# Optimization experiments

Measured on AMD Instinct MI355X. Metric: run time of the kernel, lower is better.

The kernel has to match this reference:

```python
import jax, jax.numpy as jnp
import numpy as np

N, P, C, H, W = 2, 100, 256, 128, 192
K = 3; KK = K * K; E = C * KK; NH = 8; DH = E // NH; FFN = 2048


def _ln(x, g, b, eps=1e-5):
    m = x.mean(-1, keepdims=True)
    v = ((x - m) ** 2).mean(-1, keepdims=True)
    return (x - m) * jax.lax.rsqrt(v + eps) * g + b


def setup_inputs():
    ks = iter(jax.random.split(jax.random.key(0), 64))
    def rnd(shape, s=1.0):
        return jax.random.normal(next(ks), shape, jnp.float32) * s
    z = lambda *s: jnp.zeros(s, jnp.float32)
    o = lambda *s: jnp.ones(s, jnp.float32)
    return {
        'x': rnd((N, C, H, W)),
        'proposal_feat': rnd((N, P, E)),
        'mask_preds': rnd((N, P, H, W)),
        'ku_dyn_w': rnd((2 * C, C), 0.02), 'ku_dyn_b': z(2 * C),
        'ku_in_w': rnd((2 * C, C), 0.02), 'ku_in_b': z(2 * C),
        'ku_ig_w': rnd((C, C), 0.02), 'ku_ig_b': z(C),
        'ku_ug_w': rnd((C, C), 0.02), 'ku_ug_b': z(C),
        'ku_nin_g': o(C), 'ku_nin_b': z(C),
        'ku_nout_g': o(C), 'ku_nout_b': z(C),
        'ku_inin_g': o(C), 'ku_inin_b': z(C),
        'ku_inout_g': o(C), 'ku_inout_b': z(C),
        'ku_fc_w': rnd((C, C), 0.02), 'ku_fc_b': z(C),
        'ku_fcn_g': o(C), 'ku_fcn_b': z(C),
        'attn_in_w': rnd((3 * E, E), 0.02), 'attn_in_b': z(3 * E),
        'attn_out_w': rnd((E, E), 0.02), 'attn_out_b': z(E),
        'attn_ln_g': o(E), 'attn_ln_b': z(E),
        'ffn_w1': rnd((FFN, C), 0.02), 'ffn_b1': z(FFN),
        'ffn_w2': rnd((C, FFN), 0.02), 'ffn_b2': z(C),
        'ffn_ln_g': o(C), 'ffn_ln_b': z(C),
        'mask_fc_ws': rnd((3, C, C), 0.02),
        'mask_fc_ln_g': o(3, C), 'mask_fc_ln_b': z(3, C),
        'fc_mask_w': rnd((C, C), 0.02), 'fc_mask_b': z(C),
    }


def _forward(x, proposal_feat, mask_preds, ku_dyn_w, ku_dyn_b, ku_in_w, ku_in_b,
             ku_ig_w, ku_ig_b, ku_ug_w, ku_ug_b, ku_nin_g, ku_nin_b, ku_nout_g,
             ku_nout_b, ku_inin_g, ku_inin_b, ku_inout_g, ku_inout_b, ku_fc_w,
             ku_fc_b, ku_fcn_g, ku_fcn_b, attn_in_w, attn_in_b, attn_out_w,
             attn_out_b, attn_ln_g, attn_ln_b, ffn_w1, ffn_b1, ffn_w2, ffn_b2,
             ffn_ln_g, ffn_ln_b, mask_fc_ws, mask_fc_ln_g, mask_fc_ln_b,
             fc_mask_w, fc_mask_b):
    # mask-softmax pooling over proposals: (N,P,H,W) x (N,C,H,W) -> (N,P,C)
    sig = jax.nn.softmax(mask_preds, axis=1)
    x_feat = jnp.einsum('bnhw,bchw->bnc', sig, x)

    # KernelUpdator (gated dynamic kernel update)
    pf = proposal_feat.reshape(N, P, C, KK).transpose(0, 1, 3, 2).reshape(N * P, KK, C)
    upd = x_feat.reshape(N * P, C)
    params = upd @ ku_dyn_w.T + ku_dyn_b            # (NP, 2C)
    p_in, p_out = params[:, :C], params[:, C:]
    inp = pf @ ku_in_w.T + ku_in_b                  # (NP, KK, 2C)
    i_in, i_out = inp[..., :C], inp[..., C:]
    gate = i_in * p_in[:, None, :]                  # (NP, KK, C)
    ig = jax.nn.sigmoid(_ln(gate @ ku_ig_w.T + ku_ig_b, ku_inin_g, ku_inin_b))
    ug = jax.nn.sigmoid(_ln(gate @ ku_ug_w.T + ku_ug_b, ku_nin_g, ku_nin_b))
    p_out = _ln(p_out, ku_nout_g, ku_nout_b)
    i_out = _ln(i_out, ku_inout_g, ku_inout_b)
    feat = ug * p_out[:, None, :] + ig * i_out
    feat = jax.nn.relu(_ln(feat @ ku_fc_w.T + ku_fc_b, ku_fcn_g, ku_fcn_b))  # (NP,KK,C)

    # self-attention across proposals; embed dim E = C*K*K, with residual + LN
    obj = feat.reshape(N, P, E).transpose(1, 0, 2)  # (P,N,E)
    qkv = obj @ attn_in_w.T + attn_in_b
    q, k, v = jnp.split(qkv, 3, axis=-1)
    q = q.reshape(P, N, NH, DH) * np.float32(1.0 / np.sqrt(DH))
    k = k.reshape(P, N, NH, DH)
    v = v.reshape(P, N, NH, DH)
    a = jax.nn.softmax(jnp.einsum('qnhd,knhd->nhqk', q, k), axis=-1)
    o = jnp.einsum('nhqk,knhd->qnhd', a, v).reshape(P, N, E)
    obj = _ln(obj + o @ attn_out_w.T + attn_out_b, attn_ln_g, attn_ln_b)
    obj = obj.transpose(1, 0, 2).reshape(N, P, KK, C)

    # FFN (residual) + LN, applied per (proposal, kernel position)
    h = jax.nn.relu(obj @ ffn_w1.T + ffn_b1) @ ffn_w2.T + ffn_b2
    obj = _ln(obj + h, ffn_ln_g, ffn_ln_b)

    mf = obj
    for i in range(3):
        mf = jax.nn.relu(_ln(mf @ mask_fc_ws[i].T, mask_fc_ln_g[i], mask_fc_ln_b[i]))
    mf = mf @ fc_mask_w.T + fc_mask_b               # (N,P,KK,C)
    kernels = mf.transpose(0, 1, 3, 2).reshape(N, P, C, K, K)

    # per-image dynamic conv: vmap replaces the python loop over batch
    def conv_one(xi, wi):
        return jax.lax.conv_general_dilated(
            xi[None], wi, (1, 1), 'SAME',
            dimension_numbers=('NCHW', 'OIHW', 'NCHW'))[0]
    new_masks = jax.vmap(conv_one)(x, kernels)      # (N,P,H,W)

    obj_kernels = obj.transpose(0, 1, 3, 2).reshape(N, P, C, K, K)
    return new_masks, obj_kernels


def reference(x, proposal_feat, mask_preds, ku_dyn_w, ku_dyn_b, ku_in_w, ku_in_b,
              ku_ig_w, ku_ig_b, ku_ug_w, ku_ug_b, ku_nin_g, ku_nin_b, ku_nout_g,
              ku_nout_b, ku_inin_g, ku_inin_b, ku_inout_g, ku_inout_b, ku_fc_w,
              ku_fc_b, ku_fcn_g, ku_fcn_b, attn_in_w, attn_in_b, attn_out_w,
              attn_out_b, attn_ln_g, attn_ln_b, ffn_w1, ffn_b1, ffn_w2, ffn_b2,
              ffn_ln_g, ffn_ln_b, mask_fc_ws, mask_fc_ln_g, mask_fc_ln_b,
              fc_mask_w, fc_mask_b):
    return _forward(x, proposal_feat, mask_preds, ku_dyn_w, ku_dyn_b, ku_in_w,
                    ku_in_b, ku_ig_w, ku_ig_b, ku_ug_w, ku_ug_b, ku_nin_g,
                    ku_nin_b, ku_nout_g, ku_nout_b, ku_inin_g, ku_inin_b,
                    ku_inout_g, ku_inout_b, ku_fc_w, ku_fc_b, ku_fcn_g, ku_fcn_b,
                    attn_in_w, attn_in_b, attn_out_w, attn_out_b, attn_ln_g,
                    attn_ln_b, ffn_w1, ffn_b1, ffn_w2, ffn_b2, ffn_ln_g,
                    ffn_ln_b, mask_fc_ws, mask_fc_ln_g, mask_fc_ln_b,
                    fc_mask_w, fc_mask_b)
```

## Files before the change

### kernel.cpp

```cpp
#include <hip/hip_runtime.h>
#include <hip/hip_bf16.h>

#define N_ 2
#define P_ 100
#define C_ 256
#define H_ 128
#define W_ 192
#define HW_ 24576
#define KK_ 9
#define E_ 2304
#define NH_ 8
#define DH_ 288
#define FFN_ 2048
#define NP_ 200
#define ROWS_ 1800
#define XKC_ 64

typedef __attribute__((ext_vector_type(8))) __bf16 bf16x8;
typedef __attribute__((ext_vector_type(4))) float f32x4;

__global__ __launch_bounds__(256) void k_softmax(const float* __restrict__ mp, float* __restrict__ sig){
  int idx = blockIdx.x*256 + threadIdx.x;
  if(idx >= N_*HW_) return;
  int n = idx / HW_, hw = idx - n*HW_;
  const float* base = mp + (size_t)n*P_*HW_ + hw;
  float m = -1e30f;
  for(int p=0;p<P_;p++) m = fmaxf(m, base[(size_t)p*HW_]);
  float s = 0.f;
  for(int p=0;p<P_;p++) s += __expf(base[(size_t)p*HW_] - m);
  float inv = 1.f/s;
  float* ob = sig + (size_t)n*P_*HW_ + hw;
  for(int p=0;p<P_;p++) ob[(size_t)p*HW_] = __expf(base[(size_t)p*HW_] - m)*inv;
}

__global__ __launch_bounds__(256) void k_permute_pf(const float* __restrict__ prop, float* __restrict__ pf){
  int i = blockIdx.x*256 + threadIdx.x;
  if(i >= ROWS_*C_) return;
  int c = i & 255;
  int r = i >> 8;
  int kk = r % 9, np = r / 9;
  pf[i] = prop[(size_t)np*E_ + c*KK_ + kk];
}

__global__ __launch_bounds__(256) void k_xfeat1m(const float* __restrict__ sig, const float* __restrict__ x,
                                                 float* __restrict__ partial){
  const int ct = blockIdx.x, kb = blockIdx.y, n = blockIdx.z;
  const int hw0 = kb*384;
  const int tid = threadIdx.x;
  const int wid = tid >> 6, lane = tid & 63;
  const int col = lane & 15, quad = lane >> 4;
  const int wm = wid & 1, wn = wid >> 1;
  const int MT = wm ? 3 : 4;
  __shared__ __bf16 As[112][72];
  __shared__ __bf16 Bs[128][72];
  f32x4 acc[4][4] = {};
  for(int k0=0; k0<384; k0+=64){
    __syncthreads();
    for(int i=tid; i<896; i+=256){
      int p = i >> 3, kg = i & 7;
      bf16x8 v;
      if(p < P_){
        const float* sp = &sig[((size_t)n*P_ + p)*HW_ + hw0 + k0 + kg*8];
        const float4 f0 = *(const float4*)sp;
        const float4 f1 = *(const float4*)(sp+4);
        v[0]=(__bf16)f0.x; v[1]=(__bf16)f0.y; v[2]=(__bf16)f0.z; v[3]=(__bf16)f0.w;
        v[4]=(__bf16)f1.x; v[5]=(__bf16)f1.y; v[6]=(__bf16)f1.z; v[7]=(__bf16)f1.w;
      } else {
        #pragma unroll
        for(int u=0;u<8;u++) v[u] = (__bf16)0.f;
      }
      *(bf16x8*)&As[p][kg*8] = v;
    }
    for(int i=tid; i<1024; i+=256){
      int c = i >> 3, kg = i & 7;
      const float* xp = &x[((size_t)n*C_ + ct*128 + c)*HW_ + hw0 + k0 + kg*8];
      const float4 f0 = *(const float4*)xp;
      const float4 f1 = *(const float4*)(xp+4);
      bf16x8 v;
      v[0]=(__bf16)f0.x; v[1]=(__bf16)f0.y; v[2]=(__bf16)f0.z; v[3]=(__bf16)f0.w;
      v[4]=(__bf16)f1.x; v[5]=(__bf16)f1.y; v[6]=(__bf16)f1.z; v[7]=(__bf16)f1.w;
      *(bf16x8*)&Bs[c][kg*8] = v;
    }
    __syncthreads();
    #pragma unroll
    for(int ks=0; ks<2; ks++){
      bf16x8 b[4];
      #pragma unroll
      for(int t=0;t<4;t++) b[t] = *(const bf16x8*)&Bs[(wn*4+t)*16 + col][ks*32 + quad*8];
      #pragma unroll
      for(int mt=0; mt<4; mt++){
        if(mt < MT){
          bf16x8 a = *(const bf16x8*)&As[(wm*4+mt)*16 + col][ks*32 + quad*8];
          #pragma unroll
          for(int t=0;t<4;t++)
            acc[mt][t] = __builtin_amdgcn_mfma_f32_16x16x32_bf16(a, b[t], acc[mt][t], 0, 0, 0);
        }
      }
    }
  }
  #pragma unroll
  for(int mt=0; mt<4; mt++){
    if(mt < MT){
      #pragma unroll
      for(int r=0;r<4;r++){
        int p = (wm*4+mt)*16 + quad*4 + r;
        if(p < P_){
          float* op = &partial[(((size_t)n*XKC_ + kb)*P_ + p)*C_ + ct*128 + wn*64 + col];
          #pragma unroll
          for(int t=0;t<4;t++) op[t*16] = acc[mt][t][r];
        }
      }
    }
  }
}

__global__ __launch_bounds__(256) void k_xfeat2(const float* __restrict__ partial, float* __restrict__ xfeat){
  int np = blockIdx.x;
  int n = np / P_, p = np - n*P_;
  int c = threadIdx.x;
  float s = 0.f;
  for(int kb=0;kb<XKC_;kb++) s += partial[(((size_t)n*XKC_ + kb)*P_ + p)*C_ + c];
  xfeat[(size_t)np*C_ + c] = s;
}

__global__ __launch_bounds__(256) void k_gemm_mfma(const float* __restrict__ A, const float* __restrict__ Wt,
    const float* __restrict__ bias, float* __restrict__ out, int M, int N, int K, int act)
{
  const int n0 = blockIdx.x*128, m0 = blockIdx.y*64;
  const int tid = threadIdx.x;
  const int wid = tid >> 6, lane = tid & 63;
  const int col = lane & 15, quad = lane >> 4;
  const int wm = wid & 1, wn = wid >> 1;
  __shared__ __bf16 As[64][72];
  __shared__ __bf16 Bs[128][72];
  f32x4 acc[2][4] = {};
  for(int k0=0; k0<K; k0+=64){
    __syncthreads();
    for(int i=tid; i<512; i+=256){
      int r = i >> 3, kg = i & 7;
      int m = m0 + r;
      bf16x8 v;
      if(m < M){
        const float* ap = &A[(size_t)m*K + k0 + kg*8];
        const float4 f0 = *(const float4*)ap;
        const float4 f1 = *(const float4*)(ap+4);
        v[0]=(__bf16)f0.x; v[1]=(__bf16)f0.y; v[2]=(__bf16)f0.z; v[3]=(__bf16)f0.w;
        v[4]=(__bf16)f1.x; v[5]=(__bf16)f1.y; v[6]=(__bf16)f1.z; v[7]=(__bf16)f1.w;
      } else {
        #pragma unroll
        for(int u=0;u<8;u++) v[u] = (__bf16)0.f;
      }
      *(bf16x8*)&As[r][kg*8] = v;
    }
    for(int i=tid; i<1024; i+=256){
      int r = i >> 3, kg = i & 7;
      const float* wp = &Wt[(size_t)(n0 + r)*K + k0 + kg*8];
      const float4 f0 = *(const float4*)wp;
      const float4 f1 = *(const float4*)(wp+4);
      bf16x8 v;
      v[0]=(__bf16)f0.x; v[1]=(__bf16)f0.y; v[2]=(__bf16)f0.z; v[3]=(__bf16)f0.w;
      v[4]=(__bf16)f1.x; v[5]=(__bf16)f1.y; v[6]=(__bf16)f1.z; v[7]=(__bf16)f1.w;
      *(bf16x8*)&Bs[r][kg*8] = v;
    }
    __syncthreads();
    #pragma unroll
    for(int ks=0; ks<2; ks++){
      bf16x8 b[4], a[2];
      #pragma unroll
      for(int t=0;t<4;t++) b[t] = *(const bf16x8*)&Bs[(wn*4+t)*16 + col][ks*32 + quad*8];
      #pragma unroll
      for(int mt=0;mt<2;mt++) a[mt] = *(const bf16x8*)&As[(wm*2+mt)*16 + col][ks*32 + quad*8];
      #pragma unroll
      for(int mt=0;mt<2;mt++)
        #pragma unroll
        for(int t=0;t<4;t++)
          acc[mt][t] = __builtin_amdgcn_mfma_f32_16x16x32_bf16(a[mt], b[t], acc[mt][t], 0, 0, 0);
    }
  }
  #pragma unroll
  for(int mt=0;mt<2;mt++){
    #pragma unroll
    for(int r=0;r<4;r++){
      int m = m0 + (wm*2+mt)*16 + quad*4 + r;
      if(m < M){
        #pragma unroll
        for(int t=0;t<4;t++){
          int n = n0 + (wn*4+t)*16 + col;
          float v = acc[mt][t][r];
          if(bias) v += bias[n];
          if(act == 1) v = fmaxf(v, 0.f);
          if(act == 3) ((__bf16*)out)[(size_t)m*N + n] = (__bf16)v;
          else out[(size_t)m*N + n] = v;
        }
      }
    }
  }
}

__global__ __launch_bounds__(256) void k_gemm_skM256(const float* __restrict__ A, const float* __restrict__ Wt,
    float* __restrict__ part, int M, int N, int K, int KC)
{
  const int n0 = blockIdx.x*64;
  const int kz = blockIdx.y*KC;
  const int tid = threadIdx.x;
  const int wid = tid >> 6, lane = tid & 63;
  const int col = lane & 15, quad = lane >> 4;
  const int wm = wid & 1, wn = wid >> 1;
  __shared__ __bf16 As[256][72];
  __shared__ __bf16 Bs[64][72];
  f32x4 acc[8][2] = {};
  for(int k0=kz; k0<kz+KC; k0+=64){
    __syncthreads();
    for(int i=tid; i<2048; i+=256){
      int r = i >> 3, kg = i & 7;
      bf16x8 v;
      if(r < M){
        const float* ap = &A[(size_t)r*K + k0 + kg*8];
        const float4 f0 = *(const float4*)ap;
        const float4 f1 = *(const float4*)(ap+4);
        v[0]=(__bf16)f0.x; v[1]=(__bf16)f0.y; v[2]=(__bf16)f0.z; v[3]=(__bf16)f0.w;
        v[4]=(__bf16)f1.x; v[5]=(__bf16)f1.y; v[6]=(__bf16)f1.z; v[7]=(__bf16)f1.w;
      } else {
        #pragma unroll
        for(int u=0;u<8;u++) v[u] = (__bf16)0.f;
      }
      *(bf16x8*)&As[r][kg*8] = v;
    }
    for(int i=tid; i<512; i+=256){
      int r = i >> 3, kg = i & 7;
      const float* wp = &Wt[(size_t)(n0 + r)*K + k0 + kg*8];
      const float4 f0 = *(const float4*)wp;
      const float4 f1 = *(const float4*)(wp+4);
      bf16x8 v;
      v[0]=(__bf16)f0.x; v[1]=(__bf16)f0.y; v[2]=(__bf16)f0.z; v[3]=(__bf16)f0.w;
      v[4]=(__bf16)f1.x; v[5]=(__bf16)f1.y; v[6]=(__bf16)f1.z; v[7]=(__bf16)f1.w;
      *(bf16x8*)&Bs[r][kg*8] = v;
    }
    __syncthreads();
    #pragma unroll
    for(int ks=0; ks<2; ks++){
      bf16x8 b[2];
      #pragma unroll
      for(int t=0;t<2;t++) b[t] = *(const bf16x8*)&Bs[(wn*2+t)*16 + col][ks*32 + quad*8];
      #pragma unroll
      for(int mt=0;mt<8;mt++){
        bf16x8 a = *(const bf16x8*)&As[(wm*8+mt)*16 + col][ks*32 + quad*8];
        #pragma unroll
        for(int t=0;t<2;t++)
          acc[mt][t] = __builtin_amdgcn_mfma_f32_16x16x32_bf16(a, b[t], acc[mt][t], 0, 0, 0);
      }
    }
  }
  float* pbase = part + (size_t)blockIdx.y*M*N;
  #pragma unroll
  for(int mt=0;mt<8;mt++){
    #pragma unroll
    for(int r=0;r<4;r++){
      int m = (wm*8+mt)*16 + quad*4 + r;
      if(m < M){
        #pragma unroll
        for(int t=0;t<2;t++){
          int n = n0 + (wn*2+t)*16 + col;
          pbase[(size_t)m*N + n] = acc[mt][t][r];
        }
      }
    }
  }
}

__global__ __launch_bounds__(256) void k_gemm_splitk(const float* __restrict__ A, const float* __restrict__ Wt,
    float* __restrict__ part, int M, int N, int K, int KC, int PX, int MY)
{
  const int wg = blockIdx.x;
  const int xcd = wg & 7, slot = wg >> 3;
  const int mb = slot % MY, pg = slot / MY;
  const int panel = xcd + 8*pg;
  const int PZ = K / KC;
  if(panel >= PX*PZ) return;
  const int px = panel % PX, pz = panel / PX;
  const int n0 = px*128, m0 = mb*64;
  const int kz = pz*KC;
  const int tid = threadIdx.x;
  const int wid = tid >> 6, lane = tid & 63;
  const int col = lane & 15, quad = lane >> 4;
  const int wm = wid & 1, wn = wid >> 1;
  __shared__ __bf16 As[64][72];
  __shared__ __bf16 Bs[128][72];
  f32x4 acc[2][4] = {};
  for(int k0=kz; k0<kz+KC; k0+=64){
    __syncthreads();
    for(int i=tid; i<512; i+=256){
      int r = i >> 3, kg = i & 7;
      int m = m0 + r;
      bf16x8 v;
      if(m < M){
        const float* ap = &A[(size_t)m*K + k0 + kg*8];
        const float4 f0 = *(const float4*)ap;
        const float4 f1 = *(const float4*)(ap+4);
        v[0]=(__bf16)f0.x; v[1]=(__bf16)f0.y; v[2]=(__bf16)f0.z; v[3]=(__bf16)f0.w;
        v[4]=(__bf16)f1.x; v[5]=(__bf16)f1.y; v[6]=(__bf16)f1.z; v[7]=(__bf16)f1.w;
      } else {
        #pragma unroll
        for(int u=0;u<8;u++) v[u] = (__bf16)0.f;
      }
      *(bf16x8*)&As[r][kg*8] = v;
    }
    for(int i=tid; i<1024; i+=256){
      int r = i >> 3, kg = i & 7;
      const float* wp = &Wt[(size_t)(n0 + r)*K + k0 + kg*8];
      const float4 f0 = *(const float4*)wp;
      const float4 f1 = *(const float4*)(wp+4);
      bf16x8 v;
      v[0]=(__bf16)f0.x; v[1]=(__bf16)f0.y; v[2]=(__bf16)f0.z; v[3]=(__bf16)f0.w;
      v[4]=(__bf16)f1.x; v[5]=(__bf16)f1.y; v[6]=(__bf16)f1.z; v[7]=(__bf16)f1.w;
      *(bf16x8*)&Bs[r][kg*8] = v;
    }
    __syncthreads();
    #pragma unroll
    for(int ks=0; ks<2; ks++){
      bf16x8 b[4], a[2];
      #pragma unroll
      for(int t=0;t<4;t++) b[t] = *(const bf16x8*)&Bs[(wn*4+t)*16 + col][ks*32 + quad*8];
      #pragma unroll
      for(int mt=0;mt<2;mt++) a[mt] = *(const bf16x8*)&As[(wm*2+mt)*16 + col][ks*32 + quad*8];
      #pragma unroll
      for(int mt=0;mt<2;mt++)
        #pragma unroll
        for(int t=0;t<4;t++)
          acc[mt][t] = __builtin_amdgcn_mfma_f32_16x16x32_bf16(a[mt], b[t], acc[mt][t], 0, 0, 0);
    }
  }
  float* pbase = part + (size_t)pz*M*N;
  #pragma unroll
  for(int mt=0;mt<2;mt++){
    #pragma unroll
    for(int r=0;r<4;r++){
      int m = m0 + (wm*2+mt)*16 + quad*4 + r;
      if(m < M){
        #pragma unroll
        for(int t=0;t<4;t++){
          int n = n0 + (wn*4+t)*16 + col;
          pbase[(size_t)m*N + n] = acc[mt][t][r];
        }
      }
    }
  }
}

__global__ __launch_bounds__(256) void k_redk(const float* __restrict__ part, const float* __restrict__ bias,
    float* __restrict__ out, int M, int N, int S)
{
  size_t i4 = ((size_t)blockIdx.x*256 + threadIdx.x)*4;
  size_t MN = (size_t)M*N;
  if(i4 >= MN) return;
  float4 s = *(const float4*)&part[i4];
  for(int z=1; z<S; z++){
    const float4 p = *(const float4*)&part[(size_t)z*MN + i4];
    s.x+=p.x; s.y+=p.y; s.z+=p.z; s.w+=p.w;
  }
  if(bias){
    int n = (int)(i4 % (size_t)N);
    const float4 b = *(const float4*)&bias[n];
    s.x+=b.x; s.y+=b.y; s.z+=b.z; s.w+=b.w;
  }
  *(float4*)&out[i4] = s;
}

__global__ __launch_bounds__(256) void k_ln256(const float* __restrict__ in, const float* __restrict__ res,
    const float* __restrict__ g, const float* __restrict__ b, float* __restrict__ out, int M, int act)
{
  int row = blockIdx.x*4 + (threadIdx.x >> 6);
  int lane = threadIdx.x & 63;
  if(row >= M) return;
  float4 v = *(const float4*)&in[(size_t)row*C_ + lane*4];
  if(res){
    const float4 rv = *(const float4*)&res[(size_t)row*C_ + lane*4];
    v.x += rv.x; v.y += rv.y; v.z += rv.z; v.w += rv.w;
  }
  float s = v.x + v.y + v.z + v.w;
  float q = v.x*v.x + v.y*v.y + v.z*v.z + v.w*v.w;
  #pragma unroll
  for(int off=32; off; off>>=1){ s += __shfl_xor(s, off, 64); q += __shfl_xor(q, off, 64); }
  float mean = s*(1.f/256.f);
  float rstd = rsqrtf(q*(1.f/256.f) - mean*mean + 1e-5f);
  const float4 gv = *(const float4*)&g[lane*4];
  const float4 bv = *(const float4*)&b[lane*4];
  float o[4] = {(v.x-mean)*rstd*gv.x + bv.x, (v.y-mean)*rstd*gv.y + bv.y,
                (v.z-mean)*rstd*gv.z + bv.z, (v.w-mean)*rstd*gv.w + bv.w};
  #pragma unroll
  for(int j=0;j<4;j++){
    if(act==1) o[j] = fmaxf(o[j], 0.f);
    else if(act==2) o[j] = 1.f/(1.f + __expf(-o[j]));
  }
  float4 ov = {o[0],o[1],o[2],o[3]};
  *(float4*)&out[(size_t)row*C_ + lane*4] = ov;
}

__global__ __launch_bounds__(256) void k_gate(const float* __restrict__ inp, const float* __restrict__ params,
                                              float* __restrict__ gate){
  int i = blockIdx.x*256 + threadIdx.x;
  if(i >= ROWS_*C_) return;
  int c = i & 255, r = i >> 8;
  int np = r / 9;
  gate[i] = inp[(size_t)r*512 + c] * params[(size_t)np*512 + c];
}

__device__ __forceinline__ void block_stats(float v, float* red, int slot, float& mean, float& rstd){
  float s = v, q = v*v;
  #pragma unroll
  for(int off=32; off; off>>=1){ s += __shfl_xor(s, off, 64); q += __shfl_xor(q, off, 64); }
  int wid = threadIdx.x >> 6;
  if((threadIdx.x & 63) == 0){ red[slot + wid] = s; red[slot + 4 + wid] = q; }
  __syncthreads();
  s = red[slot+0]+red[slot+1]+red[slot+2]+red[slot+3];
  q = red[slot+4]+red[slot+5]+red[slot+6]+red[slot+7];
  mean = s*(1.f/256.f);
  rstd = rsqrtf(q*(1.f/256.f) - mean*mean + 1e-5f);
}

__global__ __launch_bounds__(256) void k_combine(const float* __restrict__ params, const float* __restrict__ inp,
  const float* __restrict__ ug, const float* __restrict__ ig,
  const float* __restrict__ nout_g, const float* __restrict__ nout_b,
  const float* __restrict__ inout_g, const float* __restrict__ inout_b,
  float* __restrict__ feat)
{
  __shared__ float red[16];
  int r = blockIdx.x;
  int np = r / 9;
  int c = threadIdx.x;
  float pv = params[(size_t)np*512 + 256 + c];
  float mean, rstd;
  block_stats(pv, red, 0, mean, rstd);
  float pn = (pv - mean)*rstd*nout_g[c] + nout_b[c];
  float iv = inp[(size_t)r*512 + 256 + c];
  float mean2, rstd2;
  block_stats(iv, red, 8, mean2, rstd2);
  float iw = (iv - mean2)*rstd2*inout_g[c] + inout_b[c];
  size_t o = (size_t)r*C_ + c;
  feat[o] = ug[o]*pn + ig[o]*iw;
}

__global__ __launch_bounds__(256) void k_attn2(const float* __restrict__ qkv, float* __restrict__ attnO){
  const int qt = blockIdx.x, h = blockIdx.y, n = blockIdx.z;
  const int q0 = qt*10;
  const int tid = threadIdx.x;
  __shared__ float Qs[10][292];
  __shared__ float KVs[25][292];
  __shared__ float Ss[10][104];
  const float scale = 0.05892556509887896f;
  const size_t base = (size_t)n*P_*6912 + (size_t)h*DH_;
  for(int i=tid; i<10*DH_; i+=256){
    int qi = i/DH_, d = i - qi*DH_;
    Qs[qi][d] = qkv[base + (size_t)(q0+qi)*6912 + d] * scale;
  }
  for(int kt=0; kt<4; kt++){
    int kp0 = kt*25;
    __syncthreads();
    for(int i=tid; i<25*DH_; i+=256){
      int ki = i/DH_, d = i - ki*DH_;
      KVs[ki][d] = qkv[base + (size_t)(kp0+ki)*6912 + E_ + d];
    }
    __syncthreads();
    if(tid < 250){
      int qi = tid/25, ki = tid - qi*25;
      float s = 0.f;
      #pragma unroll 9
      for(int d=0; d<DH_; d+=4){
        const float4 a = *(const float4*)&Qs[qi][d];
        const float4 b = *(const float4*)&KVs[ki][d];
        s += a.x*b.x + a.y*b.y + a.z*b.z + a.w*b.w;
      }
      Ss[qi][kp0+ki] = s;
    }
  }
  __syncthreads();
  {
    int w = tid >> 6, lane = tid & 63;
    for(int r=w; r<10; r+=4){
      float v0 = (lane < 100) ? Ss[r][lane] : -1e30f;
      float v1 = (lane < 36)  ? Ss[r][64+lane] : -1e30f;
      float m = fmaxf(v0, v1);
      #pragma unroll
      for(int off=32; off; off>>=1) m = fmaxf(m, __shfl_xor(m, off, 64));
      float e0 = (lane < 100) ? __expf(v0-m) : 0.f;
      float e1 = (lane < 36)  ? __expf(v1-m) : 0.f;
      float s = e0 + e1;
      #pragma unroll
      for(int off=32; off; off>>=1) s += __shfl_xor(s, off, 64);
      float inv = 1.f/s;
      if(lane < 100) Ss[r][lane] = e0*inv;
      if(lane < 36)  Ss[r][64+lane] = e1*inv;
    }
  }
  float acc[12];
  #pragma unroll
  for(int j=0;j<12;j++) acc[j]=0.f;
  for(int kt=0; kt<4; kt++){
    int kp0 = kt*25;
    __syncthreads();
    for(int i=tid; i<25*DH_; i+=256){
      int ki = i/DH_, d = i - ki*DH_;
      KVs[ki][d] = qkv[base + (size_t)(kp0+ki)*6912 + 2*E_ + d];
    }
    __syncthreads();
    int j = 0;
    for(int i=tid; i<10*DH_; i+=256, j++){
      int qi = i/DH_, d = i - qi*DH_;
      float s = acc[j];
      #pragma unroll
      for(int ki=0; ki<25; ki++) s += Ss[qi][kp0+ki]*KVs[ki][d];
      acc[j] = s;
    }
  }
  {
    int j = 0;
    for(int i=tid; i<10*DH_; i+=256, j++){
      int qi = i/DH_, d = i - qi*DH_;
      attnO[(size_t)(n*P_ + q0 + qi)*E_ + h*DH_ + d] = acc[j];
    }
  }
}

__global__ __launch_bounds__(256) void k_add_ln2304(const float* __restrict__ obj0, const float* __restrict__ tp,
  const float* __restrict__ g, const float* __restrict__ b, float* __restrict__ out)
{
  __shared__ float red[8];
  int row = blockIdx.x;
  float v[9]; float s=0.f, q=0.f;
  #pragma unroll
  for(int j=0;j<9;j++){
    int e = threadIdx.x + j*256;
    float t = obj0[(size_t)row*E_ + e] + tp[(size_t)row*E_ + e];
    v[j]=t; s+=t; q+=t*t;
  }
  #pragma unroll
  for(int off=32; off; off>>=1){ s += __shfl_xor(s, off, 64); q += __shfl_xor(q, off, 64); }
  int wid = threadIdx.x>>6;
  if((threadIdx.x&63)==0){ red[wid]=s; red[4+wid]=q; }
  __syncthreads();
  s = red[0]+red[1]+red[2]+red[3]; q = red[4]+red[5]+red[6]+red[7];
  float mean = s*(1.f/2304.f);
  float rstd = rsqrtf(q*(1.f/2304.f) - mean*mean + 1e-5f);
  #pragma unroll
  for(int j=0;j<9;j++){
    int e = threadIdx.x + j*256;
    out[(size_t)row*E_ + e] = (v[j]-mean)*rstd*g[e] + b[e];
  }
}

__global__ __launch_bounds__(256) void k_objk(const float* __restrict__ obj2, float* __restrict__ outk){
  int i = blockIdx.x*256 + threadIdx.x;
  if(i >= ROWS_*C_) return;
  int kk = i % 9; int t = i / 9; int c = t & 255; int np = t >> 8;
  outk[i] = obj2[((size_t)np*9 + kk)*C_ + c];
}

__global__ __launch_bounds__(256) void k_prep_x(const float* __restrict__ x, __bf16* __restrict__ xT){
  int i = blockIdx.x*256 + threadIdx.x;
  if(i >= N_*32*H_*W_) return;
  int w = i % W_; int t = i / W_;
  int h = t % H_; t /= H_;
  int g = t % 32; int n = t / 32;
  const float* xp = &x[((size_t)(n*C_ + g*8)*H_ + h)*W_ + w];
  bf16x8 v;
  #pragma unroll
  for(int u=0;u<8;u++) v[u] = (__bf16)xp[(size_t)u*HW_];
  *(bf16x8*)&xT[(size_t)i*8] = v;
}

__global__ __launch_bounds__(256) void k_permute_ker(const __bf16* __restrict__ mfFb, __bf16* __restrict__ kerP){
  int i = blockIdx.x*256 + threadIdx.x;
  if(i >= 73728) return;
  int pl = i & 63; int t = i >> 6;
  int oct = t & 3; t >>= 2;
  int tap = t % 9; t /= 9;
  int c0b = t & 7; int nps = t >> 3;
  int n = nps >> 1, ps = nps & 1;
  int p = ps*64 + pl;
  bf16x8 v;
  if(p < P_){
    v = *(const bf16x8*)&mfFb[((size_t)(n*P_+p)*9 + tap)*C_ + c0b*32 + oct*8];
  } else {
    #pragma unroll
    for(int u=0;u<8;u++) v[u] = (__bf16)0.f;
  }
  *(bf16x8*)&kerP[(size_t)i*8] = v;
}

__global__ __launch_bounds__(256) void k_conv_mfma(const __bf16* __restrict__ xT, const __bf16* __restrict__ kerP,
                                                   float* __restrict__ out){
  const int wt = blockIdx.x, ht = blockIdx.y, z = blockIdx.z;
  const int n = z >> 1, ps = z & 1;
  const int pbase = ps*64;
  const int NT = ps ? 3 : 4;
  const int tid = threadIdx.x;
  const int hi = tid >> 6;
  const int lane = tid & 63;
  const int col = lane & 15, quad = lane >> 4;
  const int w0 = wt*64, h0 = ht*4;

  __shared__ __bf16 xs[6][4][66][8];
  __shared__ __bf16 ks[9][4][64][8];
  __bf16* ksf = &ks[0][0][0][0];

  f32x4 acc[4][4] = {};

  int xoff[7];
  __bf16* xlds[7];
  #pragma unroll
  for(int j=0;j<7;j++){
    int i = tid + j*256;
    if(i < 1584){
      int oct = i/396; int rem = i - oct*396;
      int hy = rem/66, wx = rem - hy*66;
      int hh = h0 - 1 + hy, ww = w0 - 1 + wx;
      xlds[j] = &xs[hy][oct][wx][0];
      xoff[j] = (hh>=0 && hh<H_ && ww>=0 && ww<W_) ? (((n*32+oct)*H_ + hh)*W_ + ww)*8 : -1;
    } else { xlds[j] = nullptr; xoff[j] = -1; }
  }
  const __bf16* kbase = kerP + (size_t)(n*2+ps)*8*2304*8;

  bf16x8 xv[7], kv[9];
  bf16x8 zro;
  #pragma unroll
  for(int u=0;u<8;u++) zro[u] = (__bf16)0.f;
  #pragma unroll
  for(int j=0;j<7;j++) xv[j] = zro;
  #pragma unroll
  for(int j=0;j<7;j++)
    if(xoff[j] >= 0) xv[j] = *(const bf16x8*)&xT[xoff[j]];
  #pragma unroll
  for(int j=0;j<9;j++) kv[j] = *(const bf16x8*)&kbase[(size_t)(tid + j*256)*8];

  for(int s=0; s<8; s++){
    __syncthreads();
    #pragma unroll
    for(int j=0;j<7;j++)
      if(tid + j*256 < 1584) *(bf16x8*)xlds[j] = xv[j];
    #pragma unroll
    for(int j=0;j<9;j++) *(bf16x8*)&ksf[(size_t)(tid + j*256)*8] = kv[j];
    __syncthreads();
    if(s < 7){
      #pragma unroll
      for(int j=0;j<7;j++)
        if(xoff[j] >= 0) xv[j] = *(const bf16x8*)&xT[xoff[j] + (s+1)*786432];
      const __bf16* kb2 = kbase + (size_t)(s+1)*18432;
      #pragma unroll
      for(int j=0;j<9;j++) kv[j] = *(const bf16x8*)&kb2[(size_t)(tid + j*256)*8];
    }
    #pragma unroll
    for(int ky=0; ky<3; ky++){
      #pragma unroll
      for(int kx=0; kx<3; kx++){
        const int tap = ky*3 + kx;
        const int hy = hi + ky;
        bf16x8 b[4];
        #pragma unroll
        for(int t=0;t<4;t++) b[t] = *(const bf16x8*)&xs[hy][quad][t*16 + col + kx][0];
        #pragma unroll
        for(int pt=0; pt<4; pt++){
          if(pt < NT){
            bf16x8 a = *(const bf16x8*)&ks[tap][quad][pt*16 + col][0];
            #pragma unroll
            for(int t=0;t<4;t++)
              acc[pt][t] = __builtin_amdgcn_mfma_f32_16x16x32_bf16(a, b[t], acc[pt][t], 0, 0, 0);
          }
        }
      }
    }
  }
  const int h = h0 + hi;
  #pragma unroll
  for(int pt=0; pt<4; pt++){
    if(pt < NT){
      #pragma unroll
      for(int r=0;r<4;r++){
        int p = pbase + pt*16 + quad*4 + r;
        if(p < P_){
          float* op = &out[((size_t)(n*P_+p)*H_ + h)*W_ + w0 + col];
          #pragma unroll
          for(int t=0;t<4;t++) op[t*16] = acc[pt][t][r];
        }
      }
    }
  }
}

extern "C" void kernel_launch(void* const* d_in, const int* in_sizes, int n_in,
                              void* d_out, int out_size, void* d_ws, size_t ws_size,
                              hipStream_t stream)
{
  (void)in_sizes; (void)n_in; (void)out_size; (void)ws_size;
  const float* x          = (const float*)d_in[0];
  const float* prop       = (const float*)d_in[1];
  const float* mask_pred  = (const float*)d_in[2];
  const float* ku_dyn_w   = (const float*)d_in[3];
  const float* ku_dyn_b   = (const float*)d_in[4];
  const float* ku_in_w    = (const float*)d_in[5];
  const float* ku_in_b    = (const float*)d_in[6];
  const float* ku_ig_w    = (const float*)d_in[7];
  const float* ku_ig_b    = (const float*)d_in[8];
  const float* ku_ug_w    = (const float*)d_in[9];
  const float* ku_ug_b    = (const float*)d_in[10];
  const float* ku_nin_g   = (const float*)d_in[11];
  const float* ku_nin_b   = (const float*)d_in[12];
  const float* ku_nout_g  = (const float*)d_in[13];
  const float* ku_nout_b  = (const float*)d_in[14];
  const float* ku_inin_g  = (const float*)d_in[15];
  const float* ku_inin_b  = (const float*)d_in[16];
  const float* ku_inout_g = (const float*)d_in[17];
  const float* ku_inout_b = (const float*)d_in[18];
  const float* ku_fc_w    = (const float*)d_in[19];
  const float* ku_fc_b    = (const float*)d_in[20];
  const float* ku_fcn_g   = (const float*)d_in[21];
  const float* ku_fcn_b   = (const float*)d_in[22];
  const float* attn_in_w  = (const float*)d_in[23];
  const float* attn_in_b  = (const float*)d_in[24];
  const float* attn_out_w = (const float*)d_in[25];
  const float* attn_out_b = (const float*)d_in[26];
  const float* attn_ln_g  = (const float*)d_in[27];
  const float* attn_ln_b  = (const float*)d_in[28];
  const float* ffn_w1     = (const float*)d_in[29];
  const float* ffn_b1     = (const float*)d_in[30];
  const float* ffn_w2     = (const float*)d_in[31];
  const float* ffn_b2     = (const float*)d_in[32];
  const float* ffn_ln_g   = (const float*)d_in[33];
  const float* ffn_ln_b   = (const float*)d_in[34];
  const float* mask_fc_ws = (const float*)d_in[35];
  const float* mask_fc_ln_g = (const float*)d_in[36];
  const float* mask_fc_ln_b = (const float*)d_in[37];
  const float* fc_mask_w  = (const float*)d_in[38];
  const float* fc_mask_b  = (const float*)d_in[39];

  float* ws = (float*)d_ws;
  float* sig     = ws;
  float* hbuf    = ws;
  float* skA     = ws;
  float* partial = ws + 4915200;
  float* skB     = ws + 4915200;
  float* attnO   = ws + 4915200 + 1382400;
  float* tproj   = ws + 4915200 + 1843200;
  float* tmp     = ws + 4915200 + 2304000;
  float* qkv     = ws + 8294400;
  float* xfeat   = ws + 9830400;
  float* params  = xfeat + 51200;
  float* pf      = params + 102400;
  float* inp     = pf + 460800;
  float* gate    = inp + 921600;
  float* ig      = gate + 460800;
  float* ug      = ig + 460800;
  float* feat    = ug + 460800;
  float* obj0    = feat + 460800;
  float* obj1    = obj0 + 460800;
  float* obj2    = obj1 + 460800;
  float* mf1     = obj2 + 460800;
  float* mf2     = mf1 + 460800;
  float* mfF     = mf2 + 460800;
  __bf16* xT = (__bf16*)ws;
  __bf16* kerP = (__bf16*)(ws + 6758400);

  float* out_masks = (float*)d_out;
  float* out_kern  = out_masks + (size_t)N_*P_*HW_;

  k_softmax<<<192, 256, 0, stream>>>(mask_pred, sig);
  k_permute_pf<<<1800, 256, 0, stream>>>(prop, pf);
  k_xfeat1m<<<dim3(2,XKC_,2), 256, 0, stream>>>(sig, x, partial);
  k_xfeat2<<<200, 256, 0, stream>>>(partial, xfeat);
  k_gemm_mfma<<<dim3(4,4),   256, 0, stream>>>(xfeat, ku_dyn_w, ku_dyn_b, params, 200, 512, 256, 0);
  k_gemm_mfma<<<dim3(4,29),  256, 0, stream>>>(pf, ku_in_w, ku_in_b, inp, 1800, 512, 256, 0);
  k_gate<<<1800, 256, 0, stream>>>(inp, params, gate);
  k_gemm_mfma<<<dim3(2,29),  256, 0, stream>>>(gate, ku_ig_w, ku_ig_b, tmp, 1800, 256, 256, 0);
  k_ln256<<<450, 256, 0, stream>>>(tmp, nullptr, ku_inin_g, ku_inin_b, ig, 1800, 2);
  k_gemm_mfma<<<dim3(2,29),  256, 0, stream>>>(gate, ku_ug_w, ku_ug_b, tmp, 1800, 256, 256, 0);
  k_ln256<<<450, 256, 0, stream>>>(tmp, nullptr, ku_nin_g, ku_nin_b, ug, 1800, 2);
  k_combine<<<1800, 256, 0, stream>>>(params, inp, ug, ig, ku_nout_g, ku_nout_b, ku_inout_g, ku_inout_b, feat);
  k_gemm_mfma<<<dim3(2,29),  256, 0, stream>>>(feat, ku_fc_w, ku_fc_b, tmp, 1800, 256, 256, 0);
  k_ln256<<<450, 256, 0, stream>>>(tmp, nullptr, ku_fcn_g, ku_fcn_b, obj0, 1800, 1);
  k_gemm_skM256<<<dim3(108,6), 256, 0, stream>>>(obj0, attn_in_w, skA, 200, 6912, 2304, 384);
  k_redk<<<1350, 256, 0, stream>>>(skA, attn_in_b, qkv, 200, 6912, 6);
  k_attn2<<<dim3(10,8,2), 256, 0, stream>>>(qkv, attnO);
  k_gemm_skM256<<<dim3(36,9), 256, 0, stream>>>(attnO, attn_out_w, skA, 200, 2304, 2304, 256);
  k_redk<<<450, 256, 0, stream>>>(skA, attn_out_b, tproj, 200, 2304, 9);
  k_add_ln2304<<<200, 256, 0, stream>>>(obj0, tproj, attn_ln_g, attn_ln_b, obj1);
  k_gemm_mfma<<<dim3(16,29), 256, 0, stream>>>(obj1, ffn_w1, ffn_b1, hbuf, 1800, 2048, 256, 1);
  k_gemm_splitk<<<232, 256, 0, stream>>>(hbuf, ffn_w2, skB, 1800, 256, 2048, 512, 2, 29);
  k_redk<<<450, 256, 0, stream>>>(skB, ffn_b2, tmp, 1800, 256, 4);
  k_ln256<<<450, 256, 0, stream>>>(tmp, obj1, ffn_ln_g, ffn_ln_b, obj2, 1800, 0);
  k_gemm_mfma<<<dim3(2,29),  256, 0, stream>>>(obj2, mask_fc_ws,          nullptr, tmp, 1800, 256, 256, 0);
  k_ln256<<<450, 256, 0, stream>>>(tmp, nullptr, mask_fc_ln_g,       mask_fc_ln_b,       mf1, 1800, 1);
  k_gemm_mfma<<<dim3(2,29),  256, 0, stream>>>(mf1,  mask_fc_ws + 65536,  nullptr, tmp, 1800, 256, 256, 0);
  k_ln256<<<450, 256, 0, stream>>>(tmp, nullptr, mask_fc_ln_g + 256, mask_fc_ln_b + 256, mf2, 1800, 1);
  k_gemm_mfma<<<dim3(2,29),  256, 0, stream>>>(mf2,  mask_fc_ws + 131072, nullptr, tmp, 1800, 256, 256, 0);
  k_ln256<<<450, 256, 0, stream>>>(tmp, nullptr, mask_fc_ln_g + 512, mask_fc_ln_b + 512, mf1, 1800, 1);
  k_gemm_mfma<<<dim3(2,29),  256, 0, stream>>>(mf1, fc_mask_w, fc_mask_b, mfF, 1800, 256, 256, 3);
  k_objk<<<1800, 256, 0, stream>>>(obj2, out_kern);
  k_permute_ker<<<288, 256, 0, stream>>>((const __bf16*)mfF, kerP);
  k_prep_x<<<6144, 256, 0, stream>>>(x, xT);
  k_conv_mfma<<<dim3(3,32,4), 256, 0, stream>>>(xT, kerP, out_masks);
}
```

Before: 717.0 us.

## Restructure attention as one query per wave with pre-transposed keys

Replaces the tiled attention kernel with a pre-pass that lays K out transposed (d-major, pairs of keys per lane) in workspace, followed by a kernel where each wavefront handles one query. The wave computes scores for two keys per lane with coalesced loads, does the softmax in registers via shuffles, and reads V rows straight from global memory. This removes the shared-memory K/V staging and many block-wide syncs and raises the block count from 160 to 400. In exchange it adds an extra launch and a transposed K buffer, and V is re-read from global by every query.

Measured after the change: 697.1 us. -2.8%, faster.

```diff
diff --git a/kernel.cpp b/kernel.cpp
--- a/kernel.cpp
+++ b/kernel.cpp
@@ -440,85 +440,80 @@
   feat[o] = ug[o]*pn + ig[o]*iw;
 }
 
-__global__ __launch_bounds__(256) void k_attn2(const float* __restrict__ qkv, float* __restrict__ attnO){
-  const int qt = blockIdx.x, h = blockIdx.y, n = blockIdx.z;
-  const int q0 = qt*10;
-  const int tid = threadIdx.x;
-  __shared__ float Qs[10][292];
-  __shared__ float KVs[25][292];
-  __shared__ float Ss[10][104];
+__global__ __launch_bounds__(256) void k_prep_kT(const float* __restrict__ qkv, float2* __restrict__ kT2){
+  int i = blockIdx.x*256 + threadIdx.x;
+  if(i >= N_*NH_*DH_*64) return;
+  int l = i & 63; int t = i >> 6;
+  int d = t % DH_; t /= DH_;
+  int h = t & 7, n = t >> 3;
+  float2 v = {0.f, 0.f};
+  if(l < 50){
+    size_t base = (size_t)(n*P_ + 2*l)*6912 + E_ + (size_t)h*DH_ + d;
+    v.x = qkv[base];
+    v.y = qkv[base + 6912];
+  }
+  kT2[i] = v;
+}
+
+__global__ __launch_bounds__(256) void k_attn3(const float* __restrict__ qkv, const float2* __restrict__ kT2,
+                                               float* __restrict__ attnO){
+  const int qb = blockIdx.x, h = blockIdx.y, n = blockIdx.z;
+  const int w = threadIdx.x >> 6, lane = threadIdx.x & 63;
+  const int q = qb*4 + w;
+  __shared__ float Qs[4][288];
+  __shared__ float Ps[4][128];
   const float scale = 0.05892556509887896f;
-  const size_t base = (size_t)n*P_*6912 + (size_t)h*DH_;
-  for(int i=tid; i<10*DH_; i+=256){
-    int qi = i/DH_, d = i - qi*DH_;
-    Qs[qi][d] = qkv[base + (size_t)(q0+qi)*6912 + d] * scale;
-  }
-  for(int kt=0; kt<4; kt++){
-    int kp0 = kt*25;
-    __syncthreads();
-    for(int i=tid; i<25*DH_; i+=256){
-      int ki = i/DH_, d = i - ki*DH_;
-      KVs[ki][d] = qkv[base + (size_t)(kp0+ki)*6912 + E_ + d];
-    }
-    __syncthreads();
-    if(tid < 250){
-      int qi = tid/25, ki = tid - qi*25;
-      float s = 0.f;
-      #pragma unroll 9
-      for(int d=0; d<DH_; d+=4){
-        const float4 a = *(const float4*)&Qs[qi][d];
-        const float4 b = *(const float4*)&KVs[ki][d];
-        s += a.x*b.x + a.y*b.y + a.z*b.z + a.w*b.w;
-      }
-      Ss[qi][kp0+ki] = s;
+  {
+    const float4* qrow4 = (const float4*)(qkv + (size_t)(n*P_ + q)*6912 + (size_t)h*DH_);
+    float4* qs4 = (float4*)&Qs[w][0];
+    float4 a = qrow4[lane];
+    a.x*=scale; a.y*=scale; a.z*=scale; a.w*=scale;
+    qs4[lane] = a;
+    if(lane < 8){
+      float4 b = qrow4[64+lane];
+      b.x*=scale; b.y*=scale; b.z*=scale; b.w*=scale;
+      qs4[64+lane] = b;
     }
   }
   __syncthreads();
-  {
-    int w = tid >> 6, lane = tid & 63;
-    for(int r=w; r<10; r+=4){
-      float v0 = (lane < 100) ? Ss[r][lane] : -1e30f;
-      float v1 = (lane < 36)  ? Ss[r][64+lane] : -1e30f;
-      float m = fmaxf(v0, v1);
-      #pragma unroll
-      for(int off=32; off; off>>=1) m = fmaxf(m, __shfl_xor(m, off, 64));
-      float e0 = (lane < 100) ? __expf(v0-m) : 0.f;
-      float e1 = (lane < 36)  ? __expf(v1-m) : 0.f;
-      float s = e0 + e1;
-      #pragma unroll
-      for(int off=32; off; off>>=1) s += __shfl_xor(s, off, 64);
-      float inv = 1.f/s;
-      if(lane < 100) Ss[r][lane] = e0*inv;
-      if(lane < 36)  Ss[r][64+lane] = e1*inv;
-    }
-  }
-  float acc[12];
-  #pragma unroll
-  for(int j=0;j<12;j++) acc[j]=0.f;
-  for(int kt=0; kt<4; kt++){
-    int kp0 = kt*25;
-    __syncthreads();
-    for(int i=tid; i<25*DH_; i+=256){
-      int ki = i/DH_, d = i - ki*DH_;
-      KVs[ki][d] = qkv[base + (size_t)(kp0+ki)*6912 + 2*E_ + d];
-    }
-    __syncthreads();
-    int j = 0;
-    for(int i=tid; i<10*DH_; i+=256, j++){
-      int qi = i/DH_, d = i - qi*DH_;
-      float s = acc[j];
-      #pragma unroll
-      for(int ki=0; ki<25; ki++) s += Ss[qi][kp0+ki]*KVs[ki][d];
-      acc[j] = s;
-    }
-  }
-  {
-    int j = 0;
-    for(int i=tid; i<10*DH_; i+=256, j++){
-      int qi = i/DH_, d = i - qi*DH_;
-      attnO[(size_t)(n*P_ + q0 + qi)*E_ + h*DH_ + d] = acc[j];
-    }
-  }
+  const float2* kcol = kT2 + (size_t)(n*NH_ + h)*DH_*64;
+  float s0 = 0.f, s1 = 0.f;
+  #pragma unroll 8
+  for(int d=0; d<DH_; d++){
+    float qv = Qs[w][d];
+    float2 kk = kcol[d*64 + lane];
+    s0 += qv*kk.x;
+    s1 += qv*kk.y;
+  }
+  bool valid = lane < 50;
+  float m = valid ? fmaxf(s0, s1) : -1e30f;
+  #pragma unroll
+  for(int off=32; off; off>>=1) m = fmaxf(m, __shfl_xor(m, off, 64));
+  float e0 = valid ? __expf(s0 - m) : 0.f;
+  float e1 = valid ? __expf(s1 - m) : 0.f;
+  float sum = e0 + e1;
+  #pragma unroll
+  for(int off=32; off; off>>=1) sum += __shfl_xor(sum, off, 64);
+  float inv = 1.f/sum;
+  if(valid){
+    Ps[w][2*lane]   = e0*inv;
+    Ps[w][2*lane+1] = e1*inv;
+  }
+  __syncthreads();
+  float4 accA = {0,0,0,0}, accB = {0,0,0,0};
+  const float* vbase = qkv + (size_t)n*P_*6912 + 2*E_ + (size_t)h*DH_;
+  #pragma unroll 4
+  for(int k=0; k<P_; k++){
+    float pk = Ps[w][k];
+    const float4* vr4 = (const float4*)(vbase + (size_t)k*6912);
+    float4 va = vr4[lane];
+    accA.x += pk*va.x; accA.y += pk*va.y; accA.z += pk*va.z; accA.w += pk*va.w;
+    float4 vb = vr4[64 + (lane & 7)];
+    accB.x += pk*vb.x; accB.y += pk*vb.y; accB.z += pk*vb.z; accB.w += pk*vb.w;
+  }
+  float4* orow4 = (float4*)(attnO + (size_t)(n*P_+q)*E_ + (size_t)h*DH_);
+  orow4[lane] = accA;
+  if(lane < 8) orow4[64+lane] = accB;
 }
 
 __global__ __launch_bounds__(256) void k_add_ln2304(const float* __restrict__ obj0, const float* __restrict__ tp,
@@ -736,6 +731,7 @@
   float* sig     = ws;
   float* hbuf    = ws;
   float* skA     = ws;
+  float* kT      = ws;
   float* partial = ws + 4915200;
   float* skB     = ws + 4915200;
   float* attnO   = ws + 4915200 + 1382400;
@@ -778,7 +774,8 @@
   k_ln256<<<450, 256, 0, stream>>>(tmp, nullptr, ku_fcn_g, ku_fcn_b, obj0, 1800, 1);
   k_gemm_skM256<<<dim3(108,6), 256, 0, stream>>>(obj0, attn_in_w, skA, 200, 6912, 2304, 384);
   k_redk<<<1350, 256, 0, stream>>>(skA, attn_in_b, qkv, 200, 6912, 6);
-  k_attn2<<<dim3(10,8,2), 256, 0, stream>>>(qkv, attnO);
+  k_prep_kT<<<1152, 256, 0, stream>>>(qkv, (float2*)kT);
+  k_attn3<<<dim3(25,8,2), 256, 0, stream>>>(qkv, (const float2*)kT, attnO);
   k_gemm_skM256<<<dim3(36,9), 256, 0, stream>>>(attnO, attn_out_w, skA, 200, 2304, 2304, 256);
   k_redk<<<450, 256, 0, stream>>>(skA, attn_out_b, tproj, 200, 2304, 9);
   k_add_ln2304<<<200, 256, 0, stream>>>(obj0, tproj, attn_ln_g, attn_ln_b, obj1);
```
